# Performance work log

Hardware: AMD Instinct MI355X
Metric: run time of the kernel (lower is better)

Reference implementation:

```python
import jax, jax.numpy as jnp
import numpy as np

NUM_SEGMENTS = 256


def setup_inputs() -> dict:
    key = jax.random.key(0)
    k1, k2 = jax.random.split(key)
    n, d = 1048576, 128
    inp = jax.random.normal(k1, (n, d), dtype=jnp.float32)
    batch_seg = jnp.sort(jax.random.randint(k2, (n,), 0, NUM_SEGMENTS, dtype=jnp.int32))
    return {"inp": inp, "batch_seg": batch_seg}


def reference(inp, batch_seg):
    # Segment mean: equivalent to the TF while_loop that, for each unique id,
    # gathers its rows and takes the mean. With sorted ids covering 0..B-1,
    # output row i corresponds to segment id i (order of first appearance).
    sums = jax.ops.segment_sum(inp, batch_seg, num_segments=NUM_SEGMENTS)  # (B, d)
    counts = jax.ops.segment_sum(jnp.ones((inp.shape[0],), inp.dtype), batch_seg,
                                 num_segments=NUM_SEGMENTS)  # (B,)
    counts = jnp.maximum(counts, 1)  # guard (all segments present by construction)
    return sums / counts[:, None]
```

## Files before the change

### kernel.cpp

```cpp
#include <hip/hip_runtime.h>

#define NSEG 256
#define D 128
#define COL4 (D / 4)

__global__ void init_starts_kernel(int* starts, int n) {
    int i = blockIdx.x * blockDim.x + threadIdx.x;
    if (i <= NSEG) starts[i] = n;
}

__global__ void find_starts_kernel(const int* __restrict__ seg, int n, int* __restrict__ starts) {
    int i = blockIdx.x * blockDim.x + threadIdx.x;
    if (i < n) {
        int s = seg[i];
        if (i == 0 || seg[i - 1] != s) starts[s] = i;
    }
}

__global__ __launch_bounds__(1024) void seg_mean_kernel(const float4* __restrict__ inp,
                                                        const int* __restrict__ starts,
                                                        float* __restrict__ out, int n) {
    const int s = blockIdx.x;
    __shared__ int sh_bounds[2];
    if (threadIdx.x == 0) {
        int st = starts[s];
        int en = n;
        for (int t = s + 1; t <= NSEG; ++t) {
            int v = starts[t];
            if (v < n) { en = v; break; }
        }
        sh_bounds[0] = st;
        sh_bounds[1] = en;
    }
    __syncthreads();
    const int start = sh_bounds[0];
    const int end   = sh_bounds[1];

    const int col  = threadIdx.x & (COL4 - 1);
    const int slot = threadIdx.x >> 5;

    float4 acc = make_float4(0.f, 0.f, 0.f, 0.f);
    #pragma unroll 4
    for (int r = start + slot; r < end; r += 32) {
        float4 v = inp[(size_t)r * COL4 + col];
        acc.x += v.x; acc.y += v.y; acc.z += v.z; acc.w += v.w;
    }

    __shared__ float4 red[32][COL4];
    red[slot][col] = acc;
    __syncthreads();
    #pragma unroll
    for (int stride = 16; stride >= 1; stride >>= 1) {
        if (slot < stride) {
            float4 a = red[slot][col];
            float4 b = red[slot + stride][col];
            a.x += b.x; a.y += b.y; a.z += b.z; a.w += b.w;
            red[slot][col] = a;
        }
        __syncthreads();
    }

    if (slot == 0) {
        int cnt = end - start;
        float inv = 1.0f / (float)(cnt > 1 ? cnt : 1);
        float4 a = red[0][col];
        float4 o = make_float4(a.x * inv, a.y * inv, a.z * inv, a.w * inv);
        ((float4*)out)[(size_t)s * COL4 + col] = o;
    }
}

extern "C" void kernel_launch(void* const* d_in, const int* in_sizes, int n_in,
                              void* d_out, int out_size, void* d_ws, size_t ws_size,
                              hipStream_t stream) {
    const float* inp = (const float*)d_in[0];
    const int* seg   = (const int*)d_in[1];
    float* out       = (float*)d_out;
    const int n = in_sizes[1];

    int* starts = (int*)d_ws;

    init_starts_kernel<<<2, 256, 0, stream>>>(starts, n);
    find_starts_kernel<<<(n + 255) / 256, 256, 0, stream>>>(seg, n, starts);
    seg_mean_kernel<<<NSEG, 1024, 0, stream>>>((const float4*)inp, starts, out, n);
}
```

Before: 669.7 us.

## Replace per-segment block reduction with row-chunked partial sums and atomics

Replaces the find-starts plus one-block-per-segment reduction with a grid of small blocks that each scan a fixed chunk of rows. Runs of equal segment ids are accumulated in registers and flushed to global sums and counts with atomicAdd, and a finalize kernel divides by the counts. The old version launched only 256 blocks, which underused the GPU. The new one launches about 4096 blocks to saturate memory bandwidth, at the cost of global atomics and a float summation order that is no longer deterministic.

```diff
diff --git a/kernel.cpp b/kernel.cpp
--- a/kernel.cpp
+++ b/kernel.cpp
@@ -2,70 +2,67 @@
 
 #define NSEG 256
 #define D 128
-#define COL4 (D / 4)
+#define COL4 32
+#define SLOTS 8
+#define ROWS_PER_SLOT 32
+#define ROWS_PER_BLOCK (SLOTS * ROWS_PER_SLOT)
 
-__global__ void init_starts_kernel(int* starts, int n) {
+__global__ void zero_ws_kernel(float* ws) {
     int i = blockIdx.x * blockDim.x + threadIdx.x;
-    if (i <= NSEG) starts[i] = n;
+    if (i < NSEG * D + NSEG) ws[i] = 0.f;
 }
 
-__global__ void find_starts_kernel(const int* __restrict__ seg, int n, int* __restrict__ starts) {
-    int i = blockIdx.x * blockDim.x + threadIdx.x;
-    if (i < n) {
-        int s = seg[i];
-        if (i == 0 || seg[i - 1] != s) starts[s] = i;
+__global__ __launch_bounds__(256) void partial_kernel(const float4* __restrict__ inp,
+                                                      const int* __restrict__ seg,
+                                                      float* __restrict__ sums,
+                                                      float* __restrict__ counts,
+                                                      int n) {
+    const int col  = threadIdx.x & 31;
+    const int slot = threadIdx.x >> 5;
+    const int r0 = blockIdx.x * ROWS_PER_BLOCK + slot * ROWS_PER_SLOT;
+    if (r0 >= n) return;
+    const int r1 = (r0 + ROWS_PER_SLOT < n) ? r0 + ROWS_PER_SLOT : n;
+
+    int cur = seg[r0];
+    float4 acc = make_float4(0.f, 0.f, 0.f, 0.f);
+    int runlen = 0;
+
+    #pragma unroll 4
+    for (int r = r0; r < r1; ++r) {
+        int s = seg[r];
+        float4 v = inp[(size_t)r * COL4 + col];
+        if (s != cur) {
+            float* dst = sums + (size_t)cur * D + col * 4;
+            atomicAdd(dst + 0, acc.x);
+            atomicAdd(dst + 1, acc.y);
+            atomicAdd(dst + 2, acc.z);
+            atomicAdd(dst + 3, acc.w);
+            if (col == 0) atomicAdd(counts + cur, (float)runlen);
+            cur = s;
+            acc = make_float4(0.f, 0.f, 0.f, 0.f);
+            runlen = 0;
+        }
+        acc.x += v.x; acc.y += v.y; acc.z += v.z; acc.w += v.w;
+        ++runlen;
     }
+
+    float* dst = sums + (size_t)cur * D + col * 4;
+    atomicAdd(dst + 0, acc.x);
+    atomicAdd(dst + 1, acc.y);
+    atomicAdd(dst + 2, acc.z);
+    atomicAdd(dst + 3, acc.w);
+    if (col == 0) atomicAdd(counts + cur, (float)runlen);
 }
 
-__global__ __launch_bounds__(1024) void seg_mean_kernel(const float4* __restrict__ inp,
-                                                        const int* __restrict__ starts,
-                                                        float* __restrict__ out, int n) {
-    const int s = blockIdx.x;
-    __shared__ int sh_bounds[2];
-    if (threadIdx.x == 0) {
-        int st = starts[s];
-        int en = n;
-        for (int t = s + 1; t <= NSEG; ++t) {
-            int v = starts[t];
-            if (v < n) { en = v; break; }
-        }
-        sh_bounds[0] = st;
-        sh_bounds[1] = en;
-    }
-    __syncthreads();
-    const int start = sh_bounds[0];
-    const int end   = sh_bounds[1];
-
-    const int col  = threadIdx.x & (COL4 - 1);
-    const int slot = threadIdx.x >> 5;
-
-    float4 acc = make_float4(0.f, 0.f, 0.f, 0.f);
-    #pragma unroll 4
-    for (int r = start + slot; r < end; r += 32) {
-        float4 v = inp[(size_t)r * COL4 + col];
-        acc.x += v.x; acc.y += v.y; acc.z += v.z; acc.w += v.w;
-    }
-
-    __shared__ float4 red[32][COL4];
-    red[slot][col] = acc;
-    __syncthreads();
-    #pragma unroll
-    for (int stride = 16; stride >= 1; stride >>= 1) {
-        if (slot < stride) {
-            float4 a = red[slot][col];
-            float4 b = red[slot + stride][col];
-            a.x += b.x; a.y += b.y; a.z += b.z; a.w += b.w;
-            red[slot][col] = a;
-        }
-        __syncthreads();
-    }
-
-    if (slot == 0) {
-        int cnt = end - start;
-        float inv = 1.0f / (float)(cnt > 1 ? cnt : 1);
-        float4 a = red[0][col];
-        float4 o = make_float4(a.x * inv, a.y * inv, a.z * inv, a.w * inv);
-        ((float4*)out)[(size_t)s * COL4 + col] = o;
+__global__ void finalize_kernel(const float* __restrict__ sums,
+                                const float* __restrict__ counts,
+                                float* __restrict__ out) {
+    int i = blockIdx.x * blockDim.x + threadIdx.x;
+    if (i < NSEG * D) {
+        int s = i >> 7;
+        float c = counts[s];
+        c = (c > 1.f) ? c : 1.f;
+        out[i] = sums[i] / c;
     }
 }
 
@@ -77,9 +74,13 @@
     float* out       = (float*)d_out;
     const int n = in_sizes[1];
 
-    int* starts = (int*)d_ws;
+    float* sums   = (float*)d_ws;
+    float* counts = sums + NSEG * D;
 
-    init_starts_kernel<<<2, 256, 0, stream>>>(starts, n);
-    find_starts_kernel<<<(n + 255) / 256, 256, 0, stream>>>(seg, n, starts);
-    seg_mean_kernel<<<NSEG, 1024, 0, stream>>>((const float4*)inp, starts, out, n);
+    zero_ws_kernel<<<(NSEG * D + NSEG + 255) / 256, 256, 0, stream>>>(sums);
+
+    const int nblocks = (n + ROWS_PER_BLOCK - 1) / ROWS_PER_BLOCK;
+    partial_kernel<<<nblocks, 256, 0, stream>>>((const float4*)inp, seg, sums, counts, n);
+
+    finalize_kernel<<<(NSEG * D + 255) / 256, 256, 0, stream>>>(sums, counts, out);
 }
```

Result: slower. 778.4 us (+16.2%).
